# Optimization experiments

Measured on AMD Instinct MI355X. Metric: run time of the kernel, lower is better.

The kernel has to match this reference:

```python
import jax, jax.numpy as jnp
import numpy as np

HIDDEN = 128
SIGMA_D = 0.2
SIGMA_A = 15.0
ANGLE_K = 8
FACTOR_A = 180.0 / (SIGMA_A * np.pi)


def pairwise_sqdist(x, y):
    # x: (B,N,3), y: (B,M,3) -> (B,N,M) squared distances, clamped at 0
    sq = (jnp.sum(x * x, -1)[:, :, None]
          + jnp.sum(y * y, -1)[:, None, :]
          - 2.0 * jnp.einsum('bnd,bmd->bnm', x, y))
    return jnp.maximum(sq, 0.0)


def sinusoidal_embedding(indices, d_model):
    # indices: (...,) -> (..., d_model) with interleaved sin/cos (GeoTransformer style)
    div_term = jnp.exp(jnp.arange(0, d_model, 2, dtype=indices.dtype)
                       * (-np.log(10000.0) / d_model))
    omegas = indices[..., None] * div_term  # (..., d_model/2)
    emb = jnp.stack([jnp.sin(omegas), jnp.cos(omegas)], axis=-1)
    return emb.reshape(*indices.shape, d_model)


def setup_inputs() -> dict:
    key = jax.random.key(0)
    k1, k2, k3, k4, k5 = jax.random.split(key, 5)
    B, N, H = 1, 512, HIDDEN
    bound = 1.0 / np.sqrt(H)
    return {
        'points': jax.random.normal(k1, (B, N, 3), dtype=jnp.float32),
        'Wd': jax.random.uniform(k2, (H, H), jnp.float32, -bound, bound),
        'bd': jax.random.uniform(k3, (H,), jnp.float32, -bound, bound),
        'Wa': jax.random.uniform(k4, (H, H), jnp.float32, -bound, bound),
        'ba': jax.random.uniform(k5, (H,), jnp.float32, -bound, bound),
    }


def _embedding_indices(points):
    # points: (B,N,3) -> d_indices (B,N,N), a_indices (B,N,N,k)
    B, N, _ = points.shape
    sqdist = pairwise_sqdist(points, points)
    dist_map = jnp.sqrt(sqdist)
    d_indices = dist_map / SIGMA_D
    # knn (exclude self = nearest)
    _, knn_idx = jax.lax.top_k(-dist_map, ANGLE_K + 1)  # (B,N,k+1)
    knn_idx = knn_idx[:, :, 1:]                         # (B,N,k)
    # gather neighbor coords: (B,N,k,3)
    knn_points = jax.vmap(lambda pts, idx: pts[idx])(points, knn_idx)
    ref = knn_points - points[:, :, None, :]            # (B,N,k,3)
    anc = points[:, None, :, :] - points[:, :, None, :]  # (B,N,N,3)
    ref_e = ref[:, :, None, :, :]                        # (B,N,1,k,3)
    anc_e = anc[:, :, :, None, :]                        # (B,N,N,1,3)
    cross = jnp.cross(ref_e, anc_e)                      # (B,N,N,k,3)
    sin_v = jnp.linalg.norm(cross, axis=-1)
    cos_v = jnp.sum(ref_e * anc_e, axis=-1)
    angles = jnp.arctan2(sin_v, cos_v)
    a_indices = angles * FACTOR_A
    return d_indices, a_indices


def reference(points, Wd, bd, Wa, ba):
    d_indices, a_indices = _embedding_indices(points)
    d_emb = sinusoidal_embedding(d_indices, HIDDEN)      # (B,N,N,H)
    d_emb = jnp.einsum('bnmh,gh->bnmg', d_emb, Wd) + bd
    a_emb = sinusoidal_embedding(a_indices, HIDDEN)      # (B,N,N,k,H)
    a_emb = jnp.einsum('bnmkh,gh->bnmkg', a_emb, Wa) + ba
    a_emb = jnp.max(a_emb, axis=3)                       # reduction_a == 'max'
    return d_emb + a_emb
```

## Files before the change

### kernel.cpp

```cpp
#include <hip/hip_runtime.h>
#include <math.h>

#define N_PTS 512
#define HID 128
#define KNN 8
#define MT 16
#define NTHREADS 512
#define NROWS 144

typedef __attribute__((ext_vector_type(8))) short short8_t;
typedef __attribute__((ext_vector_type(4))) float f32x4_t;

__device__ float g_refv[N_PTS * KNN * 3];
__device__ unsigned short g_wfrag[2 * 8 * 4 * 64 * 8];

__device__ __forceinline__ unsigned short f2bf(float f) {
    const unsigned int u = __float_as_uint(f);
    return (unsigned short)((u + 0x7FFFu + ((u >> 16) & 1u)) >> 16);
}

__global__ void __launch_bounds__(64) prep_kernel(
    const float* __restrict__ points, const float* __restrict__ Wd,
    const float* __restrict__ Wa)
{
    __shared__ float spts[N_PTS * 3];
    const int lane = threadIdx.x;
    const int n = blockIdx.x;

    for (int i = lane; i < N_PTS * 3; i += 64) spts[i] = points[i];
    __syncthreads();

    {
        const int idx = n * 64 + lane;
        const int sel = idx >> 14;
        const int rem = idx & 16383;
        const int gg = rem >> 7, kk = rem & 127;
        const int gtile = gg >> 4, glo = gg & 15;
        const int ktile = kk >> 5, kmid = (kk >> 3) & 3, j = kk & 7;
        const int fl = kmid * 16 + glo;
        const int dst = ((((sel * 8 + gtile) * 4 + ktile) * 64) + fl) * 8 + j;
        const float v = sel ? Wa[gg * HID + kk] : Wd[gg * HID + kk];
        g_wfrag[dst] = f2bf(v);
    }

    const float px = spts[n * 3 + 0], py = spts[n * 3 + 1], pz = spts[n * 3 + 2];
    unsigned long long keys[8];
#pragma unroll
    for (int j = 0; j < 8; ++j) {
        const int m = lane * 8 + j;
        const float dx = spts[m * 3 + 0] - px;
        const float dy = spts[m * 3 + 1] - py;
        const float dz = spts[m * 3 + 2] - pz;
        const float sq = dx * dx + dy * dy + dz * dz;
        keys[j] = ((unsigned long long)__float_as_uint(sq) << 32) | (unsigned)m;
    }
    for (int r = 0; r < 9; ++r) {
        unsigned long long lmin = ~0ULL;
#pragma unroll
        for (int j = 0; j < 8; ++j) lmin = keys[j] < lmin ? keys[j] : lmin;
        for (int s = 1; s < 64; s <<= 1) {
            const unsigned long long o = __shfl_xor(lmin, s, 64);
            lmin = o < lmin ? o : lmin;
        }
        const int mwin = (int)(unsigned)lmin;
        if ((mwin >> 3) == lane) keys[mwin & 7] = ~0ULL;
        if (r > 0 && lane == 0) {
            const int k = r - 1;
            g_refv[(n * KNN + k) * 3 + 0] = __fsub_rn(spts[mwin * 3 + 0], px);
            g_refv[(n * KNN + k) * 3 + 1] = __fsub_rn(spts[mwin * 3 + 1], py);
            g_refv[(n * KNN + k) * 3 + 2] = __fsub_rn(spts[mwin * 3 + 2], pz);
        }
    }
}

__global__ void __launch_bounds__(NTHREADS, 2) main_kernel(
    const float* __restrict__ points, const float* __restrict__ bd,
    const float* __restrict__ ba, float* __restrict__ out)
{
    __shared__ __align__(16) unsigned short sA[NROWS * HID];
    __shared__ float sBase[NROWS];
    __shared__ float sRef[KNN][3];
    __shared__ float sPm[MT][3];
    __shared__ float sPn[3];

    const int t = threadIdx.x;
    const int n = blockIdx.y;
    const int m0 = blockIdx.x * MT;

    const int r0 = t >> 6;
    const int i  = t & 63;
    const float dv2 = expf(-0.14391156831212787f * (float)i) * 0.15915494309189535f;

    if (t < 3) sPn[t] = points[n * 3 + t];
    if (t >= 64 && t < 64 + MT * 3) { int q = t - 64;  sPm[q / 3][q % 3] = points[m0 * 3 + q]; }
    if (t >= 128 && t < 128 + KNN * 3) { int q = t - 128; sRef[q / 3][q % 3] = g_refv[n * KNN * 3 + q]; }
    __syncthreads();

    if (t < MT) {
        const float qx = sPm[t][0], qy = sPm[t][1], qz = sPm[t][2];
        const float sn = __fadd_rn(__fadd_rn(__fmul_rn(sPn[0], sPn[0]), __fmul_rn(sPn[1], sPn[1])), __fmul_rn(sPn[2], sPn[2]));
        const float sm = __fadd_rn(__fadd_rn(__fmul_rn(qx, qx), __fmul_rn(qy, qy)), __fmul_rn(qz, qz));
        float dot = __fmul_rn(sPn[0], qx);
        dot = fmaf(sPn[1], qy, dot);
        dot = fmaf(sPn[2], qz, dot);
        float sq = __fsub_rn(__fadd_rn(sn, sm), __fadd_rn(dot, dot));
        sq = fmaxf(sq, 0.0f);
        sBase[t] = __fdiv_rn(__fsqrt_rn(sq), 0.2f);
    }
    if (t < MT * KNN) {
        const int pair = t >> 3, k = t & 7;
        const float ax = sPm[pair][0] - sPn[0];
        const float ay = sPm[pair][1] - sPn[1];
        const float az = sPm[pair][2] - sPn[2];
        const float rx = sRef[k][0], ry = sRef[k][1], rz = sRef[k][2];
        const float cx = ry * az - rz * ay;
        const float cy = rz * ax - rx * az;
        const float cz = rx * ay - ry * ax;
        const float sv = sqrtf(cx * cx + cy * cy + cz * cz);
        const float cv = rx * ax + ry * ay + rz * az;
        float ang;
        if (sv == 0.0f) ang = 0.0f;
        else            ang = atan2f(sv, cv);
        sBase[MT + k * 16 + pair] = ang * 3.8197186342054885f;
    }
    __syncthreads();

    {
        const float* const rd = &sBase[r0];
        char* const wr = (char*)sA + ((unsigned)((i * 4) ^ (r0 << 4)) + (unsigned)r0 * 256);
#pragma unroll
        for (int it = 0; it < 18; ++it) {
            const float base = rd[it * 8];
            const float rev0 = base * dv2;
            const float rev  = rev0 - floorf(rev0);
            const float s = __builtin_amdgcn_sinf(rev);
            const float c = __builtin_amdgcn_cosf(rev);
            const unsigned int pack = __builtin_amdgcn_perm(
                __float_as_uint(c), __float_as_uint(s), 0x07060302u);
            *(unsigned int*)(wr + it * 2048) = pack;
        }
    }
    __syncthreads();

    const int wid  = t >> 6;
    const int lane = t & 63;
    const int rlo  = lane & 15;
    const int kseg = lane >> 4;

    const short8_t* wf = (const short8_t*)g_wfrag;
    short8_t wdb[4], wab[4];
#pragma unroll
    for (int kt = 0; kt < 4; ++kt) {
        wdb[kt] = wf[(wid * 4 + kt) * 64 + lane];
        wab[kt] = wf[((8 + wid) * 4 + kt) * 64 + lane];
    }

    const char* sAb = (const char*)sA;
    f32x4_t accd = {0.f, 0.f, 0.f, 0.f};
#pragma unroll
    for (int kt = 0; kt < 4; ++kt) {
        int byte = rlo * 256 + kt * 64 + kseg * 16;
        byte ^= (rlo & 7) << 4;
        const short8_t af = *(const short8_t*)(sAb + byte);
        accd = __builtin_amdgcn_mfma_f32_16x16x32_bf16(af, wdb[kt], accd, 0, 0, 0);
    }

    f32x4_t amax = {0.f, 0.f, 0.f, 0.f};
#pragma unroll
    for (int k = 0; k < KNN; ++k) {
        f32x4_t acc = {0.f, 0.f, 0.f, 0.f};
        const int rowb = MT + k * 16 + rlo;
#pragma unroll
        for (int kt = 0; kt < 4; ++kt) {
            int byte = rowb * 256 + kt * 64 + kseg * 16;
            byte ^= (rowb & 7) << 4;
            const short8_t af = *(const short8_t*)(sAb + byte);
            acc = __builtin_amdgcn_mfma_f32_16x16x32_bf16(af, wab[kt], acc, 0, 0, 0);
        }
        if (k == 0) amax = acc;
        else {
            amax[0] = fmaxf(amax[0], acc[0]);
            amax[1] = fmaxf(amax[1], acc[1]);
            amax[2] = fmaxf(amax[2], acc[2]);
            amax[3] = fmaxf(amax[3], acc[3]);
        }
    }

    const int g = wid * 16 + rlo;
    const float bdv = bd[g];
    const float bav = ba[g];
#pragma unroll
    for (int r = 0; r < 4; ++r) {
        const int m = m0 + kseg * 4 + r;
        out[(n * N_PTS + m) * HID + g] = accd[r] + bdv + amax[r] + bav;
    }
}

extern "C" void kernel_launch(void* const* d_in, const int* in_sizes, int n_in,
                              void* d_out, int out_size, void* d_ws, size_t ws_size,
                              hipStream_t stream) {
    (void)in_sizes; (void)n_in; (void)out_size; (void)d_ws; (void)ws_size;
    const float* points = (const float*)d_in[0];
    const float* Wd     = (const float*)d_in[1];
    const float* bd     = (const float*)d_in[2];
    const float* Wa     = (const float*)d_in[3];
    const float* ba     = (const float*)d_in[4];
    float* out = (float*)d_out;

    prep_kernel<<<N_PTS, 64, 0, stream>>>(points, Wd, Wa);

    dim3 grid(N_PTS / MT, N_PTS);
    main_kernel<<<grid, NTHREADS, 0, stream>>>(points, bd, ba, out);
}
```

Measured before the change: 125.4 us.

## Halve main kernel block to 4 waves, each computing two output-column tiles

The main kernel now runs 256 threads per block instead of 512. Each wave covers two 16-wide output tiles and reuses every A fragment loaded from LDS for two MFMAs. The sin/cos staging loop is rewritten for 4 waves, with 36 iterations and an alternating XOR offset to keep the swizzled layout. This cuts LDS A reads per MFMA and lets the occupancy hint rise to 3 blocks per SM. The cost is more weight registers per thread and fewer waves per block to hide latency.

```diff
diff --git a/kernel.cpp b/kernel.cpp
--- a/kernel.cpp
+++ b/kernel.cpp
@@ -5,7 +5,7 @@
 #define HID 128
 #define KNN 8
 #define MT 16
-#define NTHREADS 512
+#define NTHREADS 256
 #define NROWS 144
 
 typedef __attribute__((ext_vector_type(8))) short short8_t;
@@ -73,7 +73,7 @@
     }
 }
 
-__global__ void __launch_bounds__(NTHREADS, 2) main_kernel(
+__global__ void __launch_bounds__(NTHREADS, 3) main_kernel(
     const float* __restrict__ points, const float* __restrict__ bd,
     const float* __restrict__ ba, float* __restrict__ out)
 {
@@ -127,17 +127,20 @@
 
     {
         const float* const rd = &sBase[r0];
-        char* const wr = (char*)sA + ((unsigned)((i * 4) ^ (r0 << 4)) + (unsigned)r0 * 256);
-#pragma unroll
-        for (int it = 0; it < 18; ++it) {
-            const float base = rd[it * 8];
+        const unsigned base0 = (unsigned)((i * 4) ^ (r0 << 4)) + (unsigned)r0 * 256;
+        char* const wr0 = (char*)sA + base0;
+        char* const wr1 = (char*)sA + (base0 ^ 64u);
+#pragma unroll
+        for (int it = 0; it < 36; ++it) {
+            const float base = rd[it * 4];
             const float rev0 = base * dv2;
             const float rev  = rev0 - floorf(rev0);
             const float s = __builtin_amdgcn_sinf(rev);
             const float c = __builtin_amdgcn_cosf(rev);
             const unsigned int pack = __builtin_amdgcn_perm(
                 __float_as_uint(c), __float_as_uint(s), 0x07060302u);
-            *(unsigned int*)(wr + it * 2048) = pack;
+            char* const wp = (it & 1) ? wr1 : wr0;
+            *(unsigned int*)(wp + it * 1024) = pack;
         }
     }
     __syncthreads();
@@ -148,51 +151,62 @@
     const int kseg = lane >> 4;
 
     const short8_t* wf = (const short8_t*)g_wfrag;
-    short8_t wdb[4], wab[4];
-#pragma unroll
-    for (int kt = 0; kt < 4; ++kt) {
-        wdb[kt] = wf[(wid * 4 + kt) * 64 + lane];
-        wab[kt] = wf[((8 + wid) * 4 + kt) * 64 + lane];
+    short8_t wdb[2][4], wab[2][4];
+#pragma unroll
+    for (int gt = 0; gt < 2; ++gt) {
+        const int gtile = wid * 2 + gt;
+#pragma unroll
+        for (int kt = 0; kt < 4; ++kt) {
+            wdb[gt][kt] = wf[(gtile * 4 + kt) * 64 + lane];
+            wab[gt][kt] = wf[((8 + gtile) * 4 + kt) * 64 + lane];
+        }
     }
 
     const char* sAb = (const char*)sA;
-    f32x4_t accd = {0.f, 0.f, 0.f, 0.f};
+    f32x4_t accd[2] = {{0.f,0.f,0.f,0.f}, {0.f,0.f,0.f,0.f}};
 #pragma unroll
     for (int kt = 0; kt < 4; ++kt) {
         int byte = rlo * 256 + kt * 64 + kseg * 16;
         byte ^= (rlo & 7) << 4;
         const short8_t af = *(const short8_t*)(sAb + byte);
-        accd = __builtin_amdgcn_mfma_f32_16x16x32_bf16(af, wdb[kt], accd, 0, 0, 0);
-    }
-
-    f32x4_t amax = {0.f, 0.f, 0.f, 0.f};
+        accd[0] = __builtin_amdgcn_mfma_f32_16x16x32_bf16(af, wdb[0][kt], accd[0], 0, 0, 0);
+        accd[1] = __builtin_amdgcn_mfma_f32_16x16x32_bf16(af, wdb[1][kt], accd[1], 0, 0, 0);
+    }
+
+    f32x4_t amax[2] = {{0.f,0.f,0.f,0.f}, {0.f,0.f,0.f,0.f}};
 #pragma unroll
     for (int k = 0; k < KNN; ++k) {
-        f32x4_t acc = {0.f, 0.f, 0.f, 0.f};
+        f32x4_t acc0 = {0.f,0.f,0.f,0.f};
+        f32x4_t acc1 = {0.f,0.f,0.f,0.f};
         const int rowb = MT + k * 16 + rlo;
 #pragma unroll
         for (int kt = 0; kt < 4; ++kt) {
             int byte = rowb * 256 + kt * 64 + kseg * 16;
             byte ^= (rowb & 7) << 4;
             const short8_t af = *(const short8_t*)(sAb + byte);
-            acc = __builtin_amdgcn_mfma_f32_16x16x32_bf16(af, wab[kt], acc, 0, 0, 0);
-        }
-        if (k == 0) amax = acc;
+            acc0 = __builtin_amdgcn_mfma_f32_16x16x32_bf16(af, wab[0][kt], acc0, 0, 0, 0);
+            acc1 = __builtin_amdgcn_mfma_f32_16x16x32_bf16(af, wab[1][kt], acc1, 0, 0, 0);
+        }
+        if (k == 0) { amax[0] = acc0; amax[1] = acc1; }
         else {
-            amax[0] = fmaxf(amax[0], acc[0]);
-            amax[1] = fmaxf(amax[1], acc[1]);
-            amax[2] = fmaxf(amax[2], acc[2]);
-            amax[3] = fmaxf(amax[3], acc[3]);
-        }
-    }
-
-    const int g = wid * 16 + rlo;
-    const float bdv = bd[g];
-    const float bav = ba[g];
-#pragma unroll
-    for (int r = 0; r < 4; ++r) {
-        const int m = m0 + kseg * 4 + r;
-        out[(n * N_PTS + m) * HID + g] = accd[r] + bdv + amax[r] + bav;
+#pragma unroll
+            for (int r = 0; r < 4; ++r) {
+                amax[0][r] = fmaxf(amax[0][r], acc0[r]);
+                amax[1][r] = fmaxf(amax[1][r], acc1[r]);
+            }
+        }
+    }
+
+#pragma unroll
+    for (int gt = 0; gt < 2; ++gt) {
+        const int g = (wid * 2 + gt) * 16 + rlo;
+        const float bdv = bd[g];
+        const float bav = ba[g];
+#pragma unroll
+        for (int r = 0; r < 4; ++r) {
+            const int m = m0 + kseg * 4 + r;
+            out[(n * N_PTS + m) * HID + g] = accd[gt][r] + bdv + amax[gt][r] + bav;
+        }
     }
 }
 
```

New measurement: 113.1 us. 9.8% less time.
